# Optimization experiments

Measured on AMD Instinct MI355X. Metric: run time of the kernel, lower is better.

The kernel has to match this reference:

```python
import jax, jax.numpy as jnp
import numpy as np
from jax import lax

# static dims (match init_kwargs)
B, F, C, H, W = 10, 64, 3, 180, 180   # batch=10 (hard-coded by reshape), arr_size frames
CH, OUT, NCLS = 64, 256, 5            # channel, out_size, len(ansmap)+1
K1, K2, POOL = 9, 5, 2                # second*diff, third, pool
EPS = 1e-5


def setup_inputs() -> dict:
    key = jax.random.key(0)
    ks = jax.random.split(key, 12)
    s = lambda k, shape: jax.random.normal(k, shape, dtype=jnp.float32) * 0.05
    return {
        "x": jax.random.normal(ks[0], (B, F, C, H, W), dtype=jnp.float32),
        "W1": s(ks[1], (CH, C, K1, K1)),
        "b1": s(ks[2], (CH,)),
        "W2": s(ks[3], (3, CH, K2, K2)),
        "b2": s(ks[4], (3,)),
        "gamma": jnp.ones((F,), jnp.float32),
        "beta": jnp.zeros((F,), jnp.float32),
        "Wih": s(ks[5], (3, OUT, 1)),
        "Whh": s(ks[6], (3, OUT, OUT)),
        "bih": s(ks[7], (3, OUT)),
        "bhh": s(ks[8], (3, OUT)),
        "Wl": s(ks[9], (NCLS, OUT)),
        "bl": s(ks[10], (NCLS,)),
    }


def _maxpool2(y):
    return lax.reduce_window(y, -jnp.inf, lax.max, (1, 1, POOL, POOL), (1, 1, POOL, POOL), 'VALID')


def reference(x, W1, b1, W2, b2, gamma, beta, Wih, Whh, bih, bhh, Wl, bl):
    # conv stack applied per frame; batch all B*F frames at once
    xc = x.reshape(B * F, C, H, W)
    y = lax.conv_general_dilated(xc, W1, (K1, K1), 'VALID') + b1[None, :, None, None]
    y = _maxpool2(jax.nn.relu(y))                      # [B*F, CH, 10, 10]
    y = lax.conv_general_dilated(y, W2, (K2, K2), 'VALID') + b2[None, :, None, None]
    y = _maxpool2(jax.nn.relu(y))                      # [B*F, 3, 1, 1]
    y = y.reshape(B, F, 3)

    # BatchNorm1d(arr_size) in train mode: normalize each of the F channels over (batch, length)
    mean = y.mean(axis=(0, 2), keepdims=True)
    var = y.var(axis=(0, 2), keepdims=True)
    y = (y - mean) / jnp.sqrt(var + EPS) * gamma[None, :, None] + beta[None, :, None]

    # per-sample reorder of the 3 channels by (max - min) range over time
    t = y.transpose(0, 2, 1)                           # [B, 3, F]
    rng = t.max(-1) - t.min(-1)                        # [B, 3]
    perm = jnp.argsort(rng, axis=1)                    # [B, 3]
    ts = jnp.take_along_axis(t, perm[:, :, None], axis=1)  # [B, 3, F]

    # rank r goes through RNN r; vmap the scan over the 3 RNNs
    seqs = ts.transpose(1, 2, 0)[..., None]            # [3, F, B, 1]

    def rnn_last(seq, wih, whh, bi, bh):               # seq: [F, B, 1]
        def step(h, xt):
            return jnp.tanh(xt @ wih.T + bi + h @ whh.T + bh), None
        h, _ = lax.scan(step, jnp.zeros((B, OUT), seq.dtype), seq)
        return h                                       # last hidden == output at t=-1

    lasts = jax.vmap(rnn_last)(seqs, Wih, Whh, bih, bhh)  # [3, B, OUT]
    avg = lasts.mean(axis=0)                           # AvgPool2d((3,1)) + Flatten -> [B, OUT]
    return avg @ Wl.T + bl                             # [B, NCLS]
```

## Files before the change

kernel.cpp:

```cpp
#include <hip/hip_runtime.h>

typedef __attribute__((ext_vector_type(8))) short bf16x8;
typedef __attribute__((ext_vector_type(4))) float f32x4;

#define MFMA16(a,b,c) __builtin_amdgcn_mfma_f32_16x16x32_bf16((a),(b),(c),0,0,0)

#define AS1 __attribute__((address_space(1)))
#define AS3 __attribute__((address_space(3)))
__device__ __forceinline__ void async16(void* lds, const void* g){
  __builtin_amdgcn_global_load_lds((const AS1 unsigned int*)g, (AS3 unsigned int*)lds, 16, 0, 0);
}

__device__ __forceinline__ unsigned short f2bf(float f){
  unsigned int u = __float_as_uint(f);
  unsigned int r = (u + 0x7fffu + ((u>>16)&1u)) >> 16;
  return (unsigned short)r;
}
__device__ __forceinline__ float bf2f(unsigned short h){
  return __uint_as_float(((unsigned int)h)<<16);
}
__device__ __forceinline__ float tanh_fast(float x){
  float e = __expf(2.f*x);
  return 1.f - 2.f/(e + 1.f);
}

#define WS_W1H   0u
#define WS_W1L   32768u
#define WS_WHHH  65536u
#define WS_WHHL  458752u
#define WS_Y1    851968u
#define WS_Y2    17235968u
#define WS_LAST  17255936u


__global__ __launch_bounds__(256) void k_prep(const float* __restrict__ W1,
                                              const float* __restrict__ Whh,
                                              unsigned short* __restrict__ w1h,
                                              unsigned short* __restrict__ w1l,
                                              unsigned short* __restrict__ whh_h,
                                              unsigned short* __restrict__ whh_l){
  int t = blockIdx.x*256 + threadIdx.x;
  if (t < 2048){
    int l = t & 63, kt = (t>>6)&7, mt = t>>9;
    int co = mt*16 + (l&15);
    int o = (kt*32 + ((l>>4)<<3)) >> 3;
    bf16x8 hv, lv;
    #pragma unroll
    for (int j=0;j<8;j++){
      float v = 0.f;
      if (o < 27){
        v = W1[co*243 + o*9 + j];
      } else if (o < 31){
        int idx = (o-27)*8 + j;
        if (idx < 27) v = W1[co*243 + idx*9 + 8];
      }
      unsigned short h = f2bf(v);
      unsigned short lo = f2bf(v - bf2f(h));
      hv[j] = (short)h; lv[j] = (short)lo;
    }
    *(bf16x8*)(w1h + (size_t)t*8) = hv;
    *(bf16x8*)(w1l + (size_t)t*8) = lv;
  } else if (t < 2048 + 24576){
    int u = t - 2048;
    int l = u & 63, kt = (u>>6)&7, nt = (u>>9)&15, rnn = u>>13;
    int o = nt*16 + (l&15);
    int k0 = kt*32 + ((l>>4)<<3);
    const float* src = Whh + ((size_t)rnn*256 + o)*256;
    bf16x8 hv, lv;
    #pragma unroll
    for (int j=0;j<8;j++){
      float v = src[k0 + j];
      unsigned short h = f2bf(v);
      unsigned short lo = f2bf(v - bf2f(h));
      hv[j] = (short)h; lv[j] = (short)lo;
    }
    *(bf16x8*)(whh_h + (size_t)u*8) = hv;
    *(bf16x8*)(whh_l + (size_t)u*8) = lv;
  }
}

__device__ __forceinline__ void load_chunk(const float* __restrict__ xf, int rowbase,
                                           int ch, float* __restrict__ f){
  int o = (ch*205)>>12;
  int p = ch - 20*o;
  if (o < 27){
    int c = (o*57)>>9;
    int ky = o - 9*c;
    const float* b = xf + c*32400 + (rowbase+ky)*180 + 9*p;
    #pragma unroll
    for (int j=0;j<8;j++) f[j] = b[j];
  } else if (o < 31){
    #pragma unroll
    for (int j=0;j<8;j++){
      int idx = (o-27)*8 + j;
      int cc = (idx*57)>>9;
      int kky = idx - 9*cc;
      f[j] = (idx<27) ? xf[cc*32400 + (rowbase+kky)*180 + 9*p + 8] : 0.f;
    }
  } else {
    #pragma unroll
    for (int j=0;j<8;j++) f[j] = 0.f;
  }
}

__device__ __forceinline__ void write_chunk(char* __restrict__ smem, int ch,
                                            const float* __restrict__ f){
  unsigned int hw[4], lw[4];
  #pragma unroll
  for (int i=0;i<4;i++){
    unsigned int ua = __float_as_uint(f[2*i]), ub = __float_as_uint(f[2*i+1]);
    float la = f[2*i]   - __uint_as_float(ua & 0xffff0000u);
    float lb = f[2*i+1] - __uint_as_float(ub & 0xffff0000u);
    hw[i] = __builtin_amdgcn_perm(ub, ua, 0x07060302u);
    lw[i] = __builtin_amdgcn_perm(__float_as_uint(lb), __float_as_uint(la), 0x07060302u);
  }
  *(uint4*)(smem + ch*16)         = make_uint4(hw[0],hw[1],hw[2],hw[3]);
  *(uint4*)(smem + 10240 + ch*16) = make_uint4(lw[0],lw[1],lw[2],lw[3]);
}

__global__ __launch_bounds__(256) void k_conv1(const float* __restrict__ x,
                                               const float* __restrict__ b1,
                                               const unsigned short* __restrict__ w1h,
                                               const unsigned short* __restrict__ w1l,
                                               float* __restrict__ y1){
  __shared__ __align__(16) char smem[20480];
  int fr = blockIdx.x/10, g = blockIdx.x%10;
  int t = threadIdx.x, w = t>>6, l = t&63;
  const float* xf = x + (size_t)fr*97200;
  int rb = g*18;

  float f0[8], f1[8], f2[8];
  load_chunk(xf, rb, t,      f0);
  load_chunk(xf, rb, t+256,  f1);
  if (t < 128) load_chunk(xf, rb, t+512, f2);

  bf16x8 ah[8], al[8];
  #pragma unroll
  for (int kt=0;kt<8;kt++){
    size_t fi = (((size_t)(w*8+kt))*64 + l)*8;
    ah[kt] = *(const bf16x8*)(w1h+fi);
    al[kt] = *(const bf16x8*)(w1l+fi);
  }
  float bias[4];
  #pragma unroll
  for (int reg=0;reg<4;reg++) bias[reg] = b1[w*16 + ((l>>4)<<2) + reg];

  write_chunk(smem, t,     f0);
  write_chunk(smem, t+256, f1);
  if (t < 128) write_chunk(smem, t+512, f2);
  __syncthreads();

  load_chunk(xf, rb+9, t,      f0);
  load_chunk(xf, rb+9, t+256,  f1);
  if (t < 128) load_chunk(xf, rb+9, t+512, f2);

  int m = l&15;
  int fb = ((l>>4)*320) + m*16;
  f32x4 acc0 = (f32x4){0.f,0.f,0.f,0.f}, acc1 = acc0;
  #pragma unroll
  for (int kt=0;kt<8;kt++){
    int off0 = fb + kt*1280;
    int off1 = off0 + 64;
    bf16x8 bh0 = *(const bf16x8*)(smem+off0);
    bf16x8 bl0 = *(const bf16x8*)(smem+10240+off0);
    bf16x8 bh1 = *(const bf16x8*)(smem+off1);
    bf16x8 bl1 = *(const bf16x8*)(smem+10240+off1);
    acc0 = MFMA16(ah[kt], bh0, acc0);
    acc0 = MFMA16(ah[kt], bl0, acc0);
    acc0 = MFMA16(al[kt], bh0, acc0);
    acc1 = MFMA16(ah[kt], bh1, acc1);
    acc1 = MFMA16(ah[kt], bl1, acc1);
    acc1 = MFMA16(al[kt], bh1, acc1);
  }
  float vA0[4], vA1[4];
  #pragma unroll
  for (int reg=0;reg<4;reg++){
    float v0 = fmaxf(acc0[reg]+bias[reg], 0.f);
    vA0[reg] = fmaxf(v0, __shfl_xor(v0,1));
    float v1 = fmaxf(acc1[reg]+bias[reg], 0.f);
    vA1[reg] = fmaxf(v1, __shfl_xor(v1,1));
  }
  __syncthreads();

  write_chunk(smem, t,     f0);
  write_chunk(smem, t+256, f1);
  if (t < 128) write_chunk(smem, t+512, f2);
  __syncthreads();

  acc0 = (f32x4){0.f,0.f,0.f,0.f}; acc1 = acc0;
  #pragma unroll
  for (int kt=0;kt<8;kt++){
    int off0 = fb + kt*1280;
    int off1 = off0 + 64;
    bf16x8 bh0 = *(const bf16x8*)(smem+off0);
    bf16x8 bl0 = *(const bf16x8*)(smem+10240+off0);
    bf16x8 bh1 = *(const bf16x8*)(smem+off1);
    bf16x8 bl1 = *(const bf16x8*)(smem+10240+off1);
    acc0 = MFMA16(ah[kt], bh0, acc0);
    acc0 = MFMA16(ah[kt], bl0, acc0);
    acc0 = MFMA16(al[kt], bh0, acc0);
    acc1 = MFMA16(ah[kt], bh1, acc1);
    acc1 = MFMA16(ah[kt], bl1, acc1);
    acc1 = MFMA16(al[kt], bh1, acc1);
  }
  size_t ybase = (size_t)fr*6400 + g*10;
  #pragma unroll
  for (int reg=0;reg<4;reg++){
    int co = w*16 + ((l>>4)<<2) + reg;
    float v0 = fmaxf(acc0[reg]+bias[reg], 0.f);
    v0 = fmaxf(v0, __shfl_xor(v0,1));
    float r0 = fmaxf(vA0[reg], v0);
    float v1 = fmaxf(acc1[reg]+bias[reg], 0.f);
    v1 = fmaxf(v1, __shfl_xor(v1,1));
    float r1 = fmaxf(vA1[reg], v1);
    if ((m&1)==0){
      y1[ybase + co*100 + (m>>1)] = r0;
      if (m >= 12)
        y1[ybase + co*100 + ((4+m)>>1)] = r1;
    }
  }
}

__global__ __launch_bounds__(256) void k_conv2(const float* __restrict__ y1,
                                               const float* __restrict__ W2,
                                               const float* __restrict__ b2,
                                               float* __restrict__ y2){
  __shared__ __align__(16) float yl[6400];
  __shared__ __align__(16) float w2s[4800];
  int fr = blockIdx.x, t = threadIdx.x;
  const float4* src = (const float4*)(y1 + (size_t)fr*6400);
  for (int i=t;i<1600;i+=256) async16(((float4*)yl) + i, (const void*)(src + i));
  for (int i=t;i<1200;i+=256) async16(((float4*)w2s) + i, (const void*)(((const float4*)W2) + i));
  __syncthreads();
  if (t < 192){
    int o = t>>4, l16 = t&15;
    int ch = o>>2, pos = o&3;
    int oy = pos>>1, ox = pos&1;
    float s = 0.f;
    for (int i=0;i<100;i++){
      int k = l16 + (i<<4);
      int ci = k/25; int r = k - ci*25; int ky = r/5, kx = r - ky*5;
      s += yl[ci*100 + (5*oy+ky)*10 + 5*ox + kx] * w2s[ch*1600 + k];
    }
    #pragma unroll
    for (int d=1; d<16; d<<=1) s += __shfl_xor(s, d);
    float v = fmaxf(s + b2[ch], 0.f);
    v = fmaxf(v, __shfl_xor(v, 16));
    v = fmaxf(v, __shfl_xor(v, 32));
    if ((t&63)==0) y2[fr*3 + (t>>6)] = v;
  }
}

__global__ __launch_bounds__(512) void k_rnn(const unsigned short* __restrict__ whh_h,
                                             const unsigned short* __restrict__ whh_l,
                                             const float* __restrict__ y2,
                                             const float* __restrict__ gamma,
                                             const float* __restrict__ beta,
                                             const float* __restrict__ Wih,
                                             const float* __restrict__ bih,
                                             const float* __restrict__ bhh,
                                             float* __restrict__ lasts){
  __shared__ __align__(16) char hsm[36864];
  float* yl   = (float*)hsm;
  float* af   = (float*)(hsm + 7680);
  float* bfv  = (float*)(hsm + 7936);
  float* rngL = (float*)(hsm + 8192);
  int*   perm = (int*)(hsm + 8320);
  float* tsb  = (float*)(hsm + 8448);
  float* seqL = (float*)(hsm + 32768);
  int rnn = blockIdx.x;
  int t = threadIdx.x, w = t>>6, l = t&63;

  bf16x8 Bh[2][8], Bl[2][8];
  #pragma unroll
  for (int q=0;q<2;q++){
    int nt = 2*w + q;
    #pragma unroll
    for (int kt=0;kt<8;kt++){
      size_t fi = (((((size_t)rnn*16 + nt)*8) + kt)*64 + l)*8;
      Bh[q][kt] = *(const bf16x8*)(whh_h + fi);
      Bl[q][kt] = *(const bf16x8*)(whh_l + fi);
    }
  }
  int o0 = (2*w)*16 + (l&15), o1 = o0 + 16;
  float wih0 = Wih[rnn*256 + o0], wih1 = Wih[rnn*256 + o1];
  float bs0 = bih[rnn*256+o0] + bhh[rnn*256+o0];
  float bs1 = bih[rnn*256+o1] + bhh[rnn*256+o1];

  for (int i=t;i<1920;i+=512) yl[i] = y2[i];
  __syncthreads();
  if (t < 64){
    float mu = 0.f;
    for (int b=0;b<10;b++)
      for (int ch=0;ch<3;ch++) mu += yl[(b*64 + t)*3 + ch];
    mu *= (1.f/30.f);
    float v = 0.f;
    for (int b=0;b<10;b++)
      for (int ch=0;ch<3;ch++){ float d = yl[(b*64+t)*3+ch] - mu; v += d*d; }
    v *= (1.f/30.f);
    float rs = rsqrtf(v + 1e-5f);
    float a = gamma[t]*rs;
    af[t] = a; bfv[t] = beta[t] - mu*a;
  }
  __syncthreads();
  if (t < 30){
    int b = t/3, ch = t - b*3;
    float mx = -1e30f, mn = 1e30f;
    for (int f=0; f<64; f++){
      float v = yl[(b*64+f)*3+ch]*af[f] + bfv[f];
      tsb[(b*3+ch)*64 + f] = v;
      mx = fmaxf(mx, v); mn = fminf(mn, v);
    }
    rngL[b*3+ch] = mx - mn;
  }
  __syncthreads();
  if (t < 10){
    #pragma unroll
    for (int ch=0; ch<3; ch++){
      float rc = rngL[t*3+ch];
      int rank = 0;
      #pragma unroll
      for (int c2=0; c2<3; c2++){
        float r2 = rngL[t*3+c2];
        if (r2 < rc || (r2 == rc && c2 < ch)) rank++;
      }
      perm[t*3+rank] = ch;
    }
  }
  __syncthreads();
  for (int i=t;i<1024;i+=512){
    int step = i>>4, b = i&15;
    float v = 0.f;
    if (b < 10){ int p = perm[b*3 + rnn]; v = tsb[(b*3+p)*64 + step]; }
    seqL[i] = v;
  }
  __syncthreads();

  float4 z4 = {0.f,0.f,0.f,0.f};
  for (int i=t; i<1024; i+=512) ((float4*)hsm)[i] = z4;
  __syncthreads();
  int arow = l&15, colb = (l>>4)<<4, sw = (arow&7)<<4;
  int b_base = (l>>4)<<2;
  for (int step=0; step<64; step++){
    char* cur = hsm + ((step&1)<<14);
    char* nxt = hsm + (((step+1)&1)<<14);
    f32x4 p0=(f32x4){0,0,0,0}, q0=p0, r0=p0, p1=p0, q1=p0, r1=p0;
    #pragma unroll
    for (int kt=0; kt<8; kt++){
      int off = ((arow<<9) + (kt<<6) + colb) ^ sw;
      bf16x8 ahv = *(const bf16x8*)(cur + off);
      bf16x8 alv = *(const bf16x8*)(cur + 8192 + off);
      p0 = MFMA16(ahv, Bh[0][kt], p0);
      q0 = MFMA16(ahv, Bl[0][kt], q0);
      r0 = MFMA16(alv, Bh[0][kt], r0);
      p1 = MFMA16(ahv, Bh[1][kt], p1);
      q1 = MFMA16(ahv, Bl[1][kt], q1);
      r1 = MFMA16(alv, Bh[1][kt], r1);
    }
    float4 sx = *(const float4*)(seqL + (step<<4) + b_base);
    float sxa[4] = {sx.x, sx.y, sx.z, sx.w};
    #pragma unroll
    for (int reg=0; reg<4; reg++){
      int b = b_base + reg;
      float a0 = (p0[reg] + q0[reg]) + r0[reg];
      float a1 = (p1[reg] + q1[reg]) + r1[reg];
      float h0 = tanh_fast(a0 + sxa[reg]*wih0 + bs0);
      float h1 = tanh_fast(a1 + sxa[reg]*wih1 + bs1);
      int wsw = (b&7)<<4;
      int off0 = ((b<<9) + (o0<<1)) ^ wsw;
      int off1 = ((b<<9) + (o1<<1)) ^ wsw;
      unsigned int u0 = __float_as_uint(h0);
      unsigned int u1 = __float_as_uint(h1);
      *(unsigned short*)(nxt + off0) = (unsigned short)(u0>>16);
      float l0 = h0 - __uint_as_float(u0 & 0xffff0000u);
      *(unsigned short*)(nxt + 8192 + off0) = (unsigned short)(__float_as_uint(l0)>>16);
      *(unsigned short*)(nxt + off1) = (unsigned short)(u1>>16);
      float l1 = h1 - __uint_as_float(u1 & 0xffff0000u);
      *(unsigned short*)(nxt + 8192 + off1) = (unsigned short)(__float_as_uint(l1)>>16);
      if (step == 63){
        lasts[((size_t)rnn*16 + b)*256 + o0] = h0;
        lasts[((size_t)rnn*16 + b)*256 + o1] = h1;
      }
    }
    __syncthreads();
  }
}

__global__ __launch_bounds__(512) void k_head(const float* __restrict__ lasts,
                                              const float* __restrict__ Wl,
                                              const float* __restrict__ bl,
                                              float* __restrict__ out){
  int t = threadIdx.x;
  if (t < 400){
    int oidx = t>>3, l8 = t&7;
    int b = oidx/5, c = oidx - b*5;
    float s = 0.f;
    for (int i=0;i<32;i++){
      int o = (l8<<5) + i;
      float avg = (lasts[(size_t)(0*16+b)*256+o] + lasts[(size_t)(1*16+b)*256+o]
                 + lasts[(size_t)(2*16+b)*256+o]) * (1.f/3.f);
      s += avg * Wl[c*256 + o];
    }
    #pragma unroll
    for (int d=1; d<8; d<<=1) s += __shfl_xor(s, d);
    if (l8 == 0) out[oidx] = s + bl[c];
  }
}

extern "C" void kernel_launch(void* const* d_in, const int* in_sizes, int n_in,
                              void* d_out, int out_size, void* d_ws, size_t ws_size,
                              hipStream_t stream){
  const float* x    = (const float*)d_in[0];
  const float* W1   = (const float*)d_in[1];
  const float* b1   = (const float*)d_in[2];
  const float* W2   = (const float*)d_in[3];
  const float* b2   = (const float*)d_in[4];
  const float* gamma= (const float*)d_in[5];
  const float* beta = (const float*)d_in[6];
  const float* Wih  = (const float*)d_in[7];
  const float* Whh  = (const float*)d_in[8];
  const float* bih  = (const float*)d_in[9];
  const float* bhh  = (const float*)d_in[10];
  const float* Wl   = (const float*)d_in[11];
  const float* bl   = (const float*)d_in[12];
  char* ws = (char*)d_ws;
  unsigned short* w1h  = (unsigned short*)(ws + WS_W1H);
  unsigned short* w1l  = (unsigned short*)(ws + WS_W1L);
  unsigned short* whhh = (unsigned short*)(ws + WS_WHHH);
  unsigned short* whhl = (unsigned short*)(ws + WS_WHHL);
  float* y1   = (float*)(ws + WS_Y1);
  float* y2   = (float*)(ws + WS_Y2);
  float* last = (float*)(ws + WS_LAST);

  hipLaunchKernelGGL(k_prep,  dim3(104),  dim3(256), 0, stream, W1, Whh, w1h, w1l, whhh, whhl);
  hipLaunchKernelGGL(k_conv1, dim3(6400), dim3(256), 0, stream, x, b1, w1h, w1l, y1);
  hipLaunchKernelGGL(k_conv2, dim3(640),  dim3(256), 0, stream, y1, W2, b2, y2);
  hipLaunchKernelGGL(k_rnn,   dim3(3),    dim3(512), 0, stream, whhh, whhl, y2, gamma, beta, Wih, bih, bhh, last);
  hipLaunchKernelGGL(k_head,  dim3(1),    dim3(512), 0, stream, last, Wl, bl, (float*)d_out);
}
```

Before: 180.4 us.

## Double-buffer conv1 row tiles and process half a frame per block

Each conv1 block now handles ten conv output rows (half a frame) instead of two, with a double-buffered LDS tile. The next row's global load is issued before the current row's MFMAs and written to the other buffer afterwards. This spreads the per-block weight-fragment loads over more work and overlaps global loads with compute. The cost is fewer blocks (1280), twice the LDS per block, and a longer serial loop per block, which may reduce occupancy and latency hiding.

```diff
diff --git a/kernel.cpp b/kernel.cpp
--- a/kernel.cpp
+++ b/kernel.cpp
@@ -103,7 +103,7 @@
   }
 }
 
-__device__ __forceinline__ void write_chunk(char* __restrict__ smem, int ch,
+__device__ __forceinline__ void write_chunk(char* __restrict__ plane, int ch,
                                             const float* __restrict__ f){
   unsigned int hw[4], lw[4];
   #pragma unroll
@@ -114,8 +114,8 @@
     hw[i] = __builtin_amdgcn_perm(ub, ua, 0x07060302u);
     lw[i] = __builtin_amdgcn_perm(__float_as_uint(lb), __float_as_uint(la), 0x07060302u);
   }
-  *(uint4*)(smem + ch*16)         = make_uint4(hw[0],hw[1],hw[2],hw[3]);
-  *(uint4*)(smem + 10240 + ch*16) = make_uint4(lw[0],lw[1],lw[2],lw[3]);
+  *(uint4*)(plane + ch*16)         = make_uint4(hw[0],hw[1],hw[2],hw[3]);
+  *(uint4*)(plane + 10240 + ch*16) = make_uint4(lw[0],lw[1],lw[2],lw[3]);
 }
 
 __global__ __launch_bounds__(256) void k_conv1(const float* __restrict__ x,
@@ -123,16 +123,16 @@
                                                const unsigned short* __restrict__ w1h,
                                                const unsigned short* __restrict__ w1l,
                                                float* __restrict__ y1){
-  __shared__ __align__(16) char smem[20480];
-  int fr = blockIdx.x/10, g = blockIdx.x%10;
+  __shared__ __align__(16) char smem[40960];
+  int fr = blockIdx.x >> 1, h = blockIdx.x & 1;
   int t = threadIdx.x, w = t>>6, l = t&63;
   const float* xf = x + (size_t)fr*97200;
-  int rb = g*18;
+  int pr0 = h*10;
 
   float f0[8], f1[8], f2[8];
-  load_chunk(xf, rb, t,      f0);
-  load_chunk(xf, rb, t+256,  f1);
-  if (t < 128) load_chunk(xf, rb, t+512, f2);
+  load_chunk(xf, pr0*9, t,     f0);
+  load_chunk(xf, pr0*9, t+256, f1);
+  if (t < 128) load_chunk(xf, pr0*9, t+512, f2);
 
   bf16x8 ah[8], al[8];
   #pragma unroll
@@ -150,74 +150,68 @@
   if (t < 128) write_chunk(smem, t+512, f2);
   __syncthreads();
 
-  load_chunk(xf, rb+9, t,      f0);
-  load_chunk(xf, rb+9, t+256,  f1);
-  if (t < 128) load_chunk(xf, rb+9, t+512, f2);
-
   int m = l&15;
   int fb = ((l>>4)*320) + m*16;
-  f32x4 acc0 = (f32x4){0.f,0.f,0.f,0.f}, acc1 = acc0;
-  #pragma unroll
-  for (int kt=0;kt<8;kt++){
-    int off0 = fb + kt*1280;
-    int off1 = off0 + 64;
-    bf16x8 bh0 = *(const bf16x8*)(smem+off0);
-    bf16x8 bl0 = *(const bf16x8*)(smem+10240+off0);
-    bf16x8 bh1 = *(const bf16x8*)(smem+off1);
-    bf16x8 bl1 = *(const bf16x8*)(smem+10240+off1);
-    acc0 = MFMA16(ah[kt], bh0, acc0);
-    acc0 = MFMA16(ah[kt], bl0, acc0);
-    acc0 = MFMA16(al[kt], bh0, acc0);
-    acc1 = MFMA16(ah[kt], bh1, acc1);
-    acc1 = MFMA16(ah[kt], bl1, acc1);
-    acc1 = MFMA16(al[kt], bh1, acc1);
-  }
   float vA0[4], vA1[4];
-  #pragma unroll
-  for (int reg=0;reg<4;reg++){
-    float v0 = fmaxf(acc0[reg]+bias[reg], 0.f);
-    vA0[reg] = fmaxf(v0, __shfl_xor(v0,1));
-    float v1 = fmaxf(acc1[reg]+bias[reg], 0.f);
-    vA1[reg] = fmaxf(v1, __shfl_xor(v1,1));
-  }
-  __syncthreads();
-
-  write_chunk(smem, t,     f0);
-  write_chunk(smem, t+256, f1);
-  if (t < 128) write_chunk(smem, t+512, f2);
-  __syncthreads();
-
-  acc0 = (f32x4){0.f,0.f,0.f,0.f}; acc1 = acc0;
-  #pragma unroll
-  for (int kt=0;kt<8;kt++){
-    int off0 = fb + kt*1280;
-    int off1 = off0 + 64;
-    bf16x8 bh0 = *(const bf16x8*)(smem+off0);
-    bf16x8 bl0 = *(const bf16x8*)(smem+10240+off0);
-    bf16x8 bh1 = *(const bf16x8*)(smem+off1);
-    bf16x8 bl1 = *(const bf16x8*)(smem+10240+off1);
-    acc0 = MFMA16(ah[kt], bh0, acc0);
-    acc0 = MFMA16(ah[kt], bl0, acc0);
-    acc0 = MFMA16(al[kt], bh0, acc0);
-    acc1 = MFMA16(ah[kt], bh1, acc1);
-    acc1 = MFMA16(ah[kt], bl1, acc1);
-    acc1 = MFMA16(al[kt], bh1, acc1);
-  }
-  size_t ybase = (size_t)fr*6400 + g*10;
-  #pragma unroll
-  for (int reg=0;reg<4;reg++){
-    int co = w*16 + ((l>>4)<<2) + reg;
-    float v0 = fmaxf(acc0[reg]+bias[reg], 0.f);
-    v0 = fmaxf(v0, __shfl_xor(v0,1));
-    float r0 = fmaxf(vA0[reg], v0);
-    float v1 = fmaxf(acc1[reg]+bias[reg], 0.f);
-    v1 = fmaxf(v1, __shfl_xor(v1,1));
-    float r1 = fmaxf(vA1[reg], v1);
-    if ((m&1)==0){
-      y1[ybase + co*100 + (m>>1)] = r0;
-      if (m >= 12)
-        y1[ybase + co*100 + ((4+m)>>1)] = r1;
-    }
+  size_t ybase = (size_t)fr*6400;
+
+  #pragma unroll 2
+  for (int r=0; r<10; ++r){
+    char* cur = smem + ((r&1)*20480);
+    char* nxt = smem + (((r+1)&1)*20480);
+    if (r < 9){
+      load_chunk(xf, (pr0+r+1)*9, t,     f0);
+      load_chunk(xf, (pr0+r+1)*9, t+256, f1);
+      if (t < 128) load_chunk(xf, (pr0+r+1)*9, t+512, f2);
+    }
+    f32x4 acc0 = (f32x4){0.f,0.f,0.f,0.f}, acc1 = acc0;
+    #pragma unroll
+    for (int kt=0;kt<8;kt++){
+      int off0 = fb + kt*1280;
+      int off1 = off0 + 64;
+      bf16x8 bh0 = *(const bf16x8*)(cur+off0);
+      bf16x8 bl0 = *(const bf16x8*)(cur+10240+off0);
+      bf16x8 bh1 = *(const bf16x8*)(cur+off1);
+      bf16x8 bl1 = *(const bf16x8*)(cur+10240+off1);
+      acc0 = MFMA16(ah[kt], bh0, acc0);
+      acc0 = MFMA16(ah[kt], bl0, acc0);
+      acc0 = MFMA16(al[kt], bh0, acc0);
+      acc1 = MFMA16(ah[kt], bh1, acc1);
+      acc1 = MFMA16(ah[kt], bl1, acc1);
+      acc1 = MFMA16(al[kt], bh1, acc1);
+    }
+    if ((r&1)==0){
+      #pragma unroll
+      for (int reg=0;reg<4;reg++){
+        float v0 = fmaxf(acc0[reg]+bias[reg], 0.f);
+        vA0[reg] = fmaxf(v0, __shfl_xor(v0,1));
+        float v1 = fmaxf(acc1[reg]+bias[reg], 0.f);
+        vA1[reg] = fmaxf(v1, __shfl_xor(v1,1));
+      }
+    } else {
+      int g = h*5 + (r>>1);
+      #pragma unroll
+      for (int reg=0;reg<4;reg++){
+        int co = w*16 + ((l>>4)<<2) + reg;
+        float v0 = fmaxf(acc0[reg]+bias[reg], 0.f);
+        v0 = fmaxf(v0, __shfl_xor(v0,1));
+        float r0v = fmaxf(vA0[reg], v0);
+        float v1 = fmaxf(acc1[reg]+bias[reg], 0.f);
+        v1 = fmaxf(v1, __shfl_xor(v1,1));
+        float r1v = fmaxf(vA1[reg], v1);
+        if ((m&1)==0){
+          y1[ybase + co*100 + g*10 + (m>>1)] = r0v;
+          if (m >= 12)
+            y1[ybase + co*100 + g*10 + ((4+m)>>1)] = r1v;
+        }
+      }
+    }
+    if (r < 9){
+      write_chunk(nxt, t,     f0);
+      write_chunk(nxt, t+256, f1);
+      if (t < 128) write_chunk(nxt, t+512, f2);
+    }
+    __syncthreads();
   }
 }
 
@@ -433,7 +427,7 @@
   float* last = (float*)(ws + WS_LAST);
 
   hipLaunchKernelGGL(k_prep,  dim3(104),  dim3(256), 0, stream, W1, Whh, w1h, w1l, whhh, whhl);
-  hipLaunchKernelGGL(k_conv1, dim3(6400), dim3(256), 0, stream, x, b1, w1h, w1l, y1);
+  hipLaunchKernelGGL(k_conv1, dim3(1280), dim3(256), 0, stream, x, b1, w1h, w1l, y1);
   hipLaunchKernelGGL(k_conv2, dim3(640),  dim3(256), 0, stream, y1, W2, b2, y2);
   hipLaunchKernelGGL(k_rnn,   dim3(3),    dim3(512), 0, stream, whhh, whhl, y2, gamma, beta, Wih, bih, bhh, last);
   hipLaunchKernelGGL(k_head,  dim3(1),    dim3(512), 0, stream, last, Wl, bl, (float*)d_out);
```

Result: slower. 208.0 us (+15.3%).
